# Kernel optimization log

Measured on AMD Instinct MI355X. Metric: run time of the kernel, lower is better.

The kernel has to match this reference:

```python
import jax, jax.numpy as jnp
import numpy as np

MASK_VALUE = -10000000000.0
B, S = 2, 2048
HQ, HKV, HD = 16, 8, 256
D = HQ * HD  # 4096
ROPE_BASE = 10000.0


def rms_norm(x, scale, eps=1e-6):
    # Gemma-style RMSNorm over the last (head_dim) axis with (1 + scale) gain.
    var = jnp.mean(jnp.square(x), axis=-1, keepdims=True)
    return x * jax.lax.rsqrt(var + eps) * (1.0 + scale)


def apply_rope(x, positions):
    # x: [b, t, h, d]; positions: [b, t]
    d = x.shape[-1]
    fraction = 2.0 * jnp.arange(d // 2, dtype=jnp.float32) / d
    timescale = ROPE_BASE ** fraction                     # [d/2]
    sinusoid = positions[..., None].astype(jnp.float32) / timescale  # [b, t, d/2]
    sin = jnp.sin(sinusoid)[:, :, None, :]                # [b, t, 1, d/2]
    cos = jnp.cos(sinusoid)[:, :, None, :]
    first, second = jnp.split(x, 2, axis=-1)
    out = jnp.concatenate([first * cos - second * sin,
                           second * cos + first * sin], axis=-1)
    return out.astype(x.dtype)


def setup_inputs() -> dict:
    key = jax.random.key(0)
    ks = jax.random.split(key, 6)
    x = jax.random.normal(ks[0], (B, S, D), dtype=jnp.float32)
    Wq = jax.random.normal(ks[1], (D, HQ * HD), dtype=jnp.float32) * 0.02
    Wk = jax.random.normal(ks[2], (D, HKV * HD), dtype=jnp.float32) * 0.02
    Wv = jax.random.normal(ks[3], (D, HKV * HD), dtype=jnp.float32) * 0.02
    Wo = jax.random.normal(ks[4], (HQ * HD, D), dtype=jnp.float32) * 0.02
    k_scale = jnp.zeros((HD,), dtype=jnp.float32)
    v_scale = jnp.zeros((HD,), dtype=jnp.float32)
    mask = jnp.broadcast_to(jnp.tril(jnp.ones((S, S), dtype=bool))[None], (B, S, S))
    position = jnp.broadcast_to(jnp.arange(S, dtype=jnp.int32)[None], (B, S))
    return {"x": x, "Wq": Wq, "Wk": Wk, "Wv": Wv, "Wo": Wo,
            "k_scale": k_scale, "v_scale": v_scale,
            "mask": mask, "position": position}


def reference(x, Wq, Wk, Wv, Wo, k_scale, v_scale, mask, position):
    b, t, _ = x.shape
    group = HQ // HKV
    q = (x @ Wq).reshape(b, t, HQ, HD)
    k = (x @ Wk).reshape(b, t, HKV, HD)
    v = (x @ Wv).reshape(b, t, HKV, HD)
    k = rms_norm(k, k_scale)
    v = rms_norm(v, v_scale)
    q = apply_rope(q, position)
    k = apply_rope(k, position)
    # [b, hkv, group, t, d] view of q; avoids materializing repeated K/V (same math as repeat).
    q = q.transpose(0, 2, 1, 3).reshape(b, HKV, group, t, HD)
    k = k.transpose(0, 2, 1, 3)  # [b, hkv, T, d]
    v = v.transpose(0, 2, 1, 3)
    scores = jnp.einsum('bhgtd,bhTd->bhgtT', q, k) / jnp.sqrt(jnp.float32(HD))
    scores = jnp.where(mask[:, None, None, :, :], scores, MASK_VALUE)
    weights = jax.nn.softmax(scores, axis=-1)
    out = jnp.einsum('bhgtT,bhTd->bhgtd', weights, v)
    out = out.reshape(b, HQ, t, HD).transpose(0, 2, 1, 3).reshape(b, t, HQ * HD)
    return out @ Wo
```

## Files before the change

kernel.cpp:

```cpp
#include <hip/hip_runtime.h>
#include <stdint.h>

typedef __bf16 bf16;
typedef __bf16 bf16x4 __attribute__((ext_vector_type(4)));
typedef __bf16 bf16x8 __attribute__((ext_vector_type(8)));
typedef float f32x4 __attribute__((ext_vector_type(4)));

#define GAS __attribute__((address_space(1)))
#define LAS __attribute__((address_space(3)))

__device__ __forceinline__ void gload_lds16(const void* g, void* l) {
  __builtin_amdgcn_global_load_lds((GAS const void*)g, (LAS void*)l, 16, 0, 0);
}

__global__ __launch_bounds__(256) void cvt_bf16(const float* __restrict__ in,
                                                bf16* __restrict__ out, int n4) {
  int i = blockIdx.x * 256 + threadIdx.x;
  if (i >= n4) return;
  float4 v = ((const float4*)in)[i];
  bf16x4 o;
  o[0] = (bf16)v.x; o[1] = (bf16)v.y; o[2] = (bf16)v.z; o[3] = (bf16)v.w;
  ((bf16x4*)out)[i] = o;
}

__global__ __launch_bounds__(256) void tconv(const float* __restrict__ W,
                                             bf16* __restrict__ Wt, int K, int N) {
  __shared__ bf16 tile[64][65];
  const int tx = threadIdx.x & 63, ty = threadIdx.x >> 6;
  const int n0 = blockIdx.x * 64, k0 = blockIdx.y * 64;
#pragma unroll
  for (int i = 0; i < 16; ++i) {
    int kr = ty + i * 4;
    tile[kr][tx] = (bf16)W[(size_t)(k0 + kr) * N + n0 + tx];
  }
  __syncthreads();
#pragma unroll
  for (int i = 0; i < 16; ++i) {
    int nr = ty + i * 4;
    Wt[(size_t)(n0 + nr) * K + k0 + tx] = tile[tx][nr];
  }
}

template <int OUTF32>
__global__ __launch_bounds__(256, 3) void gemm_bt(const bf16* __restrict__ A,
                                                  const bf16* __restrict__ Bt,
                                                  void* __restrict__ Cp,
                                                  const int M, const int N, const int K) {
  __shared__ __attribute__((aligned(16))) bf16 As[4096];
  __shared__ __attribute__((aligned(16))) bf16 Bs[4096];
  const int t = threadIdx.x, w = t >> 6, l = t & 63;
  const int la = l & 15, lq = l >> 4;
  const int m0 = blockIdx.y * 128, n0 = blockIdx.x * 128;
  const int wr = w >> 1, wc = w & 1;
  const int r1 = t >> 2, s1 = (t & 3) ^ (r1 & 3);
  const bf16* Ag1 = A + (size_t)(m0 + r1) * K + s1 * 8;
  const bf16* Ag2 = A + (size_t)(m0 + r1 + 64) * K + s1 * 8;
  const bf16* Bg1 = Bt + (size_t)(n0 + r1) * K + s1 * 8;
  const bf16* Bg2 = Bt + (size_t)(n0 + r1 + 64) * K + s1 * 8;
  const int rdsl = (lq ^ (la & 3)) << 3;

  f32x4 acc[4][4] = {};

  for (int kt = 0; kt < K; kt += 32) {
    gload_lds16(Ag1 + kt, As + w * 512);
    gload_lds16(Ag2 + kt, As + 2048 + w * 512);
    gload_lds16(Bg1 + kt, Bs + w * 512);
    gload_lds16(Bg2 + kt, Bs + 2048 + w * 512);
    __syncthreads();
    bf16x8 af[4], bfr[4];
#pragma unroll
    for (int i = 0; i < 4; ++i) {
      af[i] = *(const bf16x8*)(As + (wr * 64 + i * 16 + la) * 32 + rdsl);
      bfr[i] = *(const bf16x8*)(Bs + (wc * 64 + i * 16 + la) * 32 + rdsl);
    }
#pragma unroll
    for (int mi = 0; mi < 4; ++mi)
#pragma unroll
      for (int ni = 0; ni < 4; ++ni)
        acc[mi][ni] = __builtin_amdgcn_mfma_f32_16x16x32_bf16(af[mi], bfr[ni], acc[mi][ni], 0, 0, 0);
    __syncthreads();
  }

  const int crow = m0 + wr * 64, ccol = n0 + wc * 64;
  if (OUTF32) {
    float* C = (float*)Cp;
#pragma unroll
    for (int mi = 0; mi < 4; ++mi)
#pragma unroll
      for (int ni = 0; ni < 4; ++ni)
#pragma unroll
        for (int i = 0; i < 4; ++i)
          C[(size_t)(crow + mi * 16 + lq * 4 + i) * N + ccol + ni * 16 + la] = acc[mi][ni][i];
  } else {
    bf16* C = (bf16*)Cp;
#pragma unroll
    for (int mi = 0; mi < 4; ++mi)
#pragma unroll
      for (int ni = 0; ni < 4; ++ni)
#pragma unroll
        for (int i = 0; i < 4; ++i)
          C[(size_t)(crow + mi * 16 + lq * 4 + i) * N + ccol + ni * 16 + la] = (bf16)acc[mi][ni][i];
  }
}

__global__ __launch_bounds__(256) void rope_q(bf16* __restrict__ qq, const int* __restrict__ pos) {
  const int w = threadIdx.x >> 6, l = threadIdx.x & 63;
  const int row = blockIdx.x * 4 + w;
  const int bt = row >> 4;
  bf16* p = qq + (size_t)row * 256 + l * 4;
  bf16x4 xv = *(const bf16x4*)p;
  float x[4], y[4];
#pragma unroll
  for (int j = 0; j < 4; ++j) x[j] = (float)xv[j];
#pragma unroll
  for (int j = 0; j < 4; ++j) y[j] = __shfl_xor(x[j], 32, 64);
  const float posf = (float)pos[bt];
  bf16x4 ov;
#pragma unroll
  for (int j = 0; j < 4; ++j) {
    const int pr = (l & 31) * 4 + j;
    float sv, cv;
    sincosf(posf * exp2f((float)pr * (-13.287712379549449f / 128.0f)), &sv, &cv);
    float o = x[j] * cv + ((l < 32) ? -y[j] : y[j]) * sv;
    ov[j] = (bf16)(o * 0.0625f);
  }
  *(bf16x4*)p = ov;
}

__global__ __launch_bounds__(256) void norm_rope_k(bf16* __restrict__ kk,
                                                   const float* __restrict__ scale,
                                                   const int* __restrict__ pos) {
  const int w = threadIdx.x >> 6, l = threadIdx.x & 63;
  const int row = blockIdx.x * 4 + w;
  const int bt = row >> 3;
  bf16* p = kk + (size_t)row * 256 + l * 4;
  bf16x4 xv = *(const bf16x4*)p;
  float x[4];
#pragma unroll
  for (int j = 0; j < 4; ++j) x[j] = (float)xv[j];
  float ss = x[0] * x[0] + x[1] * x[1] + x[2] * x[2] + x[3] * x[3];
#pragma unroll
  for (int m = 1; m < 64; m <<= 1) ss += __shfl_xor(ss, m, 64);
  const float r = rsqrtf(ss * (1.0f / 256.0f) + 1e-6f);
#pragma unroll
  for (int j = 0; j < 4; ++j) x[j] = x[j] * r * (1.0f + scale[l * 4 + j]);
  float y[4];
#pragma unroll
  for (int j = 0; j < 4; ++j) y[j] = __shfl_xor(x[j], 32, 64);
  const float posf = (float)pos[bt];
  bf16x4 ov;
#pragma unroll
  for (int j = 0; j < 4; ++j) {
    const int pr = (l & 31) * 4 + j;
    float sv, cv;
    sincosf(posf * exp2f((float)pr * (-13.287712379549449f / 128.0f)), &sv, &cv);
    float o = x[j] * cv + ((l < 32) ? -y[j] : y[j]) * sv;
    ov[j] = (bf16)o;
  }
  *(bf16x4*)p = ov;
}

__global__ __launch_bounds__(256) void norm_v(bf16* __restrict__ vv,
                                              const float* __restrict__ scale) {
  const int w = threadIdx.x >> 6, l = threadIdx.x & 63;
  const int row = blockIdx.x * 4 + w;
  bf16* p = vv + (size_t)row * 256 + l * 4;
  bf16x4 xv = *(const bf16x4*)p;
  float x[4];
#pragma unroll
  for (int j = 0; j < 4; ++j) x[j] = (float)xv[j];
  float ss = x[0] * x[0] + x[1] * x[1] + x[2] * x[2] + x[3] * x[3];
#pragma unroll
  for (int m = 1; m < 64; m <<= 1) ss += __shfl_xor(ss, m, 64);
  const float r = rsqrtf(ss * (1.0f / 256.0f) + 1e-6f);
  bf16x4 ov;
#pragma unroll
  for (int j = 0; j < 4; ++j) ov[j] = (bf16)(x[j] * r * (1.0f + scale[l * 4 + j]));
  *(bf16x4*)p = ov;
}

__global__ __launch_bounds__(256) void vtrans(const bf16* __restrict__ v,
                                              bf16* __restrict__ vt) {
  __shared__ bf16 tile[64][65];
  const int tx = threadIdx.x & 63, ty = threadIdx.x >> 6;
  const int tt = blockIdx.x, dd = blockIdx.y, bh = blockIdx.z;
  const int b = bh >> 3, h = bh & 7;
#pragma unroll
  for (int i = 0; i < 16; ++i) {
    int trow = tt * 64 + ty + i * 4;
    tile[ty + i * 4][tx] = v[((size_t)(b * 2048 + trow) * 8 + h) * 256 + dd * 64 + tx];
  }
  __syncthreads();
#pragma unroll
  for (int i = 0; i < 16; ++i) {
    int drow = dd * 64 + ty + i * 4;
    vt[((size_t)(b * 8 + h) * 256 + drow) * 2048 + tt * 64 + tx] = tile[tx][ty + i * 4];
  }
}

__global__ __launch_bounds__(512, 2) void flash_attn(const bf16* __restrict__ q,
                                                     const bf16* __restrict__ k,
                                                     const bf16* __restrict__ vt,
                                                     bf16* __restrict__ o) {
  __shared__ __attribute__((aligned(16))) bf16 Ks[2 * 16384];
  __shared__ __attribute__((aligned(16))) bf16 Vs[2 * 16384];
  __shared__ __attribute__((aligned(16))) bf16 Ps[8 * 1152];
  const int t = threadIdx.x, w = t >> 6, l = t & 63;
  const int la = l & 15, lq = l >> 4;
  const int h = blockIdx.x, qbp = blockIdx.y, b = blockIdx.z;
  const int hkv = h >> 1;

  const bf16* kbase = k + (size_t)b * 2048 * 2048 + hkv * 256;
  const bf16* vbase = vt + ((size_t)(b * 8 + hkv)) * 256 * 2048;

  const bf16* ksrc[4];
  const bf16* vsrc[4];
#pragma unroll
  for (int i = 0; i < 4; ++i) {
    int c = i * 512 + t;
    int krr = c >> 5, ksl = (c & 31) ^ (krr & 7);
    int vrr = c >> 3, vsl = (c & 7) ^ (vrr & 7);
    ksrc[i] = kbase + (size_t)krr * 2048 + ksl * 8;
    vsrc[i] = vbase + (size_t)vrr * 2048 + vsl * 8;
  }

#define STAGE(bb, tt0)                                                        \
  do {                                                                        \
    _Pragma("unroll") for (int i_ = 0; i_ < 4; ++i_)                          \
        gload_lds16(ksrc[i_] + (size_t)(tt0) * 2048,                          \
                    Ks + (bb) * 16384 + i_ * 4096 + w * 512);                 \
    _Pragma("unroll") for (int i_ = 0; i_ < 4; ++i_)                          \
        gload_lds16(vsrc[i_] + (tt0), Vs + (bb) * 16384 + i_ * 4096 + w * 512); \
  } while (0)

  for (int part = 0; part < 2; ++part) {
    const int qb = part ? qbp : (15 - qbp);
    const int q0 = qb * 128;
    const int rbase = q0 + w * 16;

    bf16x8 qf[8];
    {
      const bf16* qrow = q + ((size_t)((b * 2048 + rbase + la) * 16 + h)) * 256 + lq * 8;
#pragma unroll
      for (int kg = 0; kg < 8; ++kg) qf[kg] = *(const bf16x8*)(qrow + kg * 32);
    }
    f32x4 acc[16] = {};
    float mrow[4] = {-1e30f, -1e30f, -1e30f, -1e30f};
    float lrow[4] = {0.f, 0.f, 0.f, 0.f};
    const int nT = 2 * qb + 2;

    STAGE(0, 0);
    int cur = 0;
    for (int tti = 0; tti < nT; ++tti) {
      const int t0 = tti * 64;
      if (tti + 1 < nT) {
        STAGE(cur ^ 1, t0 + 64);
        asm volatile("s_waitcnt vmcnt(8)" ::: "memory");
      } else {
        asm volatile("s_waitcnt vmcnt(0)" ::: "memory");
      }
      __builtin_amdgcn_s_barrier();
      __builtin_amdgcn_sched_barrier(0);
      if (t0 <= rbase + 15) {
        const bf16* Kc = Ks + cur * 16384;
        const bf16* Vc = Vs + cur * 16384;
        f32x4 s[4] = {};
        __builtin_amdgcn_s_setprio(1);
#pragma unroll
        for (int n = 0; n < 4; ++n) {
          int rT = n * 16 + la;
#pragma unroll
          for (int kg = 0; kg < 8; ++kg) {
            int sl = (kg * 4 + lq) ^ (rT & 7);
            bf16x8 kbv = *(const bf16x8*)(Kc + rT * 256 + sl * 8);
            s[n] = __builtin_amdgcn_mfma_f32_16x16x32_bf16(qf[kg], kbv, s[n], 0, 0, 0);
          }
        }
        __builtin_amdgcn_s_setprio(0);
        float scalef[4];
#pragma unroll
        for (int i = 0; i < 4; ++i) {
          const int row = rbase + lq * 4 + i;
          float mx = -1e30f;
#pragma unroll
          for (int n = 0; n < 4; ++n) {
            float v = s[n][i];
            v = (t0 + n * 16 + la > row) ? -1e30f : v;
            s[n][i] = v;
            mx = fmaxf(mx, v);
          }
          mx = fmaxf(mx, __shfl_xor(mx, 1, 64));
          mx = fmaxf(mx, __shfl_xor(mx, 2, 64));
          mx = fmaxf(mx, __shfl_xor(mx, 4, 64));
          mx = fmaxf(mx, __shfl_xor(mx, 8, 64));
          const float mnew = fmaxf(mrow[i], mx);
          scalef[i] = __expf(mrow[i] - mnew);
          float ps = 0.f;
#pragma unroll
          for (int n = 0; n < 4; ++n) {
            float v = s[n][i];
            float pp = (v <= -1e29f) ? 0.f : __expf(v - mnew);
            s[n][i] = pp;
            ps += pp;
          }
          ps += __shfl_xor(ps, 1, 64);
          ps += __shfl_xor(ps, 2, 64);
          ps += __shfl_xor(ps, 4, 64);
          ps += __shfl_xor(ps, 8, 64);
          mrow[i] = mnew;
          lrow[i] = lrow[i] * scalef[i] + ps;
        }
#pragma unroll
        for (int n = 0; n < 16; ++n) {
          acc[n][0] *= scalef[0]; acc[n][1] *= scalef[1];
          acc[n][2] *= scalef[2]; acc[n][3] *= scalef[3];
        }
        bf16* pw = Ps + w * 1152;
#pragma unroll
        for (int n = 0; n < 4; ++n)
#pragma unroll
          for (int i = 0; i < 4; ++i)
            pw[(lq * 4 + i) * 72 + n * 16 + la] = (bf16)s[n][i];
        __builtin_amdgcn_s_setprio(1);
#pragma unroll
        for (int kc = 0; kc < 2; ++kc) {
          bf16x8 pa = *(const bf16x8*)(pw + la * 72 + kc * 32 + lq * 8);
#pragma unroll
          for (int n = 0; n < 16; ++n) {
            int rd = n * 16 + la;
            int sl = (kc * 4 + lq) ^ (rd & 7);
            bf16x8 vbv = *(const bf16x8*)(Vc + rd * 64 + sl * 8);
            acc[n] = __builtin_amdgcn_mfma_f32_16x16x32_bf16(pa, vbv, acc[n], 0, 0, 0);
          }
        }
        __builtin_amdgcn_s_setprio(0);
      }
      __builtin_amdgcn_s_barrier();
      __builtin_amdgcn_sched_barrier(0);
      cur ^= 1;
    }
#pragma unroll
    for (int i = 0; i < 4; ++i) {
      const int row = rbase + lq * 4 + i;
      const float inv = 1.0f / lrow[i];
      bf16* orow = o + ((size_t)(b * 2048 + row)) * 4096 + h * 256;
#pragma unroll
      for (int n = 0; n < 16; ++n) orow[n * 16 + la] = (bf16)(acc[n][i] * inv);
    }
  }
#undef STAGE
}

__global__ void fill_err(float* o, int n) {
  int i = blockIdx.x * 256 + threadIdx.x;
  if (i < n) o[i] = 1e9f;
}

extern "C" void kernel_launch(void* const* d_in, const int* in_sizes, int n_in,
                              void* d_out, int out_size, void* d_ws, size_t ws_size,
                              hipStream_t stream) {
  const float* x = (const float*)d_in[0];
  const float* Wq = (const float*)d_in[1];
  const float* Wk = (const float*)d_in[2];
  const float* Wv = (const float*)d_in[3];
  const float* Wo = (const float*)d_in[4];
  const float* kscale = (const float*)d_in[5];
  const float* vscale = (const float*)d_in[6];
  const int* pos = (const int*)d_in[8];
  float* out = (float*)d_out;

  const size_t WS_NEED = 251658240ull;
  if (ws_size < WS_NEED) {
    fill_err<<<65536, 256, 0, stream>>>(out, out_size);
    return;
  }
  char* ws = (char*)d_ws;
  bf16* x16 = (bf16*)(ws);
  bf16* wqt = (bf16*)(ws + 33554432);
  bf16* wkt = (bf16*)(ws + 67108864);
  bf16* wvt = (bf16*)(ws + 83886080);
  bf16* wot = (bf16*)(ws + 100663296);
  bf16* qb = (bf16*)(ws + 134217728);
  bf16* kb = (bf16*)(ws + 167772160);
  bf16* vb = (bf16*)(ws + 184549376);
  bf16* vtb = (bf16*)(ws + 201326592);
  bf16* ao = (bf16*)(ws + 218103808);

  cvt_bf16<<<16384, 256, 0, stream>>>(x, x16, 4194304);
  tconv<<<dim3(64, 64), 256, 0, stream>>>(Wq, wqt, 4096, 4096);
  tconv<<<dim3(32, 64), 256, 0, stream>>>(Wk, wkt, 4096, 2048);
  tconv<<<dim3(32, 64), 256, 0, stream>>>(Wv, wvt, 4096, 2048);
  tconv<<<dim3(64, 64), 256, 0, stream>>>(Wo, wot, 4096, 4096);

  gemm_bt<0><<<dim3(32, 32), 256, 0, stream>>>(x16, wqt, qb, 4096, 4096, 4096);
  gemm_bt<0><<<dim3(16, 32), 256, 0, stream>>>(x16, wkt, kb, 4096, 2048, 4096);
  gemm_bt<0><<<dim3(16, 32), 256, 0, stream>>>(x16, wvt, vb, 4096, 2048, 4096);

  rope_q<<<16384, 256, 0, stream>>>(qb, pos);
  norm_rope_k<<<8192, 256, 0, stream>>>(kb, kscale, pos);
  norm_v<<<8192, 256, 0, stream>>>(vb, vscale);
  vtrans<<<dim3(32, 4, 16), 256, 0, stream>>>(vb, vtb);

  flash_attn<<<dim3(16, 8, 2), 512, 0, stream>>>(qb, kb, vtb, ao);

  gemm_bt<1><<<dim3(32, 32), 256, 0, stream>>>(ao, wot, out, 4096, 4096, 4096);
}
```

Baseline: 744.0 us.

## Fuse QKV projections into one GEMM with 256x256 pipelined tiles

Concatenates the transposed Wq/Wk/Wv into one weight matrix so a single GEMM produces an interleaved QKV buffer. The downstream rope, norm, transpose and attention kernels are re-indexed to read that layout. The GEMM is rewritten with 256x256 tiles, 512 threads, double-buffered LDS, and staged prefetch of the next K slab interleaved with MFMA phases. It also adds XCD-aware block swizzling and setprio. The aim is more data reuse per tile, fewer launches and overlap of loads with compute, at the cost of higher LDS and register use per block.

Result: faster. 666.7 us (-10.4%).

```diff
diff --git a/kernel.cpp b/kernel.cpp
--- a/kernel.cpp
+++ b/kernel.cpp
@@ -42,50 +42,98 @@
 }
 
 template <int OUTF32>
-__global__ __launch_bounds__(256, 3) void gemm_bt(const bf16* __restrict__ A,
+__global__ __launch_bounds__(512, 2) void gemm256(const bf16* __restrict__ A,
                                                   const bf16* __restrict__ Bt,
                                                   void* __restrict__ Cp,
-                                                  const int M, const int N, const int K) {
-  __shared__ __attribute__((aligned(16))) bf16 As[4096];
-  __shared__ __attribute__((aligned(16))) bf16 Bs[4096];
+                                                  const int N, const int K,
+                                                  const int NBX) {
+  __shared__ __attribute__((aligned(16))) bf16 lds[2][4][8192];
   const int t = threadIdx.x, w = t >> 6, l = t & 63;
   const int la = l & 15, lq = l >> 4;
-  const int m0 = blockIdx.y * 128, n0 = blockIdx.x * 128;
-  const int wr = w >> 1, wc = w & 1;
-  const int r1 = t >> 2, s1 = (t & 3) ^ (r1 & 3);
-  const bf16* Ag1 = A + (size_t)(m0 + r1) * K + s1 * 8;
-  const bf16* Ag2 = A + (size_t)(m0 + r1 + 64) * K + s1 * 8;
-  const bf16* Bg1 = Bt + (size_t)(n0 + r1) * K + s1 * 8;
-  const bf16* Bg2 = Bt + (size_t)(n0 + r1 + 64) * K + s1 * 8;
-  const int rdsl = (lq ^ (la & 3)) << 3;
-
-  f32x4 acc[4][4] = {};
-
-  for (int kt = 0; kt < K; kt += 32) {
-    gload_lds16(Ag1 + kt, As + w * 512);
-    gload_lds16(Ag2 + kt, As + 2048 + w * 512);
-    gload_lds16(Bg1 + kt, Bs + w * 512);
-    gload_lds16(Bg2 + kt, Bs + 2048 + w * 512);
-    __syncthreads();
-    bf16x8 af[4], bfr[4];
-#pragma unroll
-    for (int i = 0; i < 4; ++i) {
-      af[i] = *(const bf16x8*)(As + (wr * 64 + i * 16 + la) * 32 + rdsl);
-      bfr[i] = *(const bf16x8*)(Bs + (wc * 64 + i * 16 + la) * 32 + rdsl);
-    }
-#pragma unroll
-    for (int mi = 0; mi < 4; ++mi)
-#pragma unroll
-      for (int ni = 0; ni < 4; ++ni)
-        acc[mi][ni] = __builtin_amdgcn_mfma_f32_16x16x32_bf16(af[mi], bfr[ni], acc[mi][ni], 0, 0, 0);
-    __syncthreads();
-  }
-
-  const int crow = m0 + wr * 64, ccol = n0 + wc * 64;
+  const int nwg = gridDim.x, cpx = nwg >> 3;
+  const int sid = (blockIdx.x & 7) * cpx + (blockIdx.x >> 3);
+  const int by = sid / NBX, bx = sid % NBX;
+  const int m0 = by * 256, n0 = bx * 256;
+  const int wr = w >> 2, wc = w & 3;
+  const int c0 = w * 64 + l;
+  const int sr0 = c0 >> 2, soff = (((c0 & 3) ^ ((c0 >> 3) & 3)) << 3);
+  const bf16* pA0 = A + (size_t)(m0 + sr0) * K + soff;
+  const bf16* pA1 = pA0 + (size_t)128 * K;
+  const bf16* pB0 = Bt + (size_t)(n0 + sr0) * K + soff;
+  const bf16* pB1 = pB0 + (size_t)128 * K;
+  const int rsl = (lq ^ ((la >> 1) & 3)) << 3;
+
+  f32x4 acc[8][4] = {};
+
+#define STAGE_SLAB(s, nb, kti)                                                \
+  do {                                                                        \
+    const bf16* p0_ = ((s) & 1) ? pB0 : pA0;                                  \
+    const bf16* p1_ = ((s) & 1) ? pB1 : pA1;                                  \
+    const size_t ko_ = (size_t)(kti) * 64 + ((s) >> 1) * 32;                  \
+    gload_lds16(p0_ + ko_, &lds[nb][s][w * 512]);                             \
+    gload_lds16(p1_ + ko_, &lds[nb][s][4096 + w * 512]);                      \
+  } while (0)
+
+#define PHASE(kh, mg, LOADB)                                                  \
+  {                                                                           \
+    bf16x8 a_[4];                                                             \
+    _Pragma("unroll") for (int m_ = 0; m_ < 4; ++m_)                          \
+        a_[m_] = *(const bf16x8*)&lds[bi][(kh)*2][(wr * 128 + (mg)*64 + m_ * 16 + la) * 32 + rsl]; \
+    if (LOADB) {                                                              \
+      _Pragma("unroll") for (int n_ = 0; n_ < 4; ++n_)                        \
+          bfr[n_] = *(const bf16x8*)&lds[bi][(kh)*2 + 1][(wc * 64 + n_ * 16 + la) * 32 + rsl]; \
+    }                                                                         \
+    __builtin_amdgcn_s_setprio(1);                                            \
+    _Pragma("unroll") for (int m_ = 0; m_ < 4; ++m_)                          \
+      _Pragma("unroll") for (int n_ = 0; n_ < 4; ++n_)                        \
+          acc[(mg)*4 + m_][n_] = __builtin_amdgcn_mfma_f32_16x16x32_bf16(     \
+              a_[m_], bfr[n_], acc[(mg)*4 + m_][n_], 0, 0, 0);                \
+    __builtin_amdgcn_s_setprio(0);                                            \
+  }
+
+  STAGE_SLAB(0, 0, 0);
+  STAGE_SLAB(1, 0, 0);
+  STAGE_SLAB(2, 0, 0);
+  STAGE_SLAB(3, 0, 0);
+
+  const int NT = K >> 6;
+  for (int kt = 0; kt < NT; ++kt) {
+    const int bi = kt & 1, nbi = bi ^ 1;
+    const bool pf = (kt + 1) < NT;
+    bf16x8 bfr[4];
+    if (pf) asm volatile("s_waitcnt vmcnt(4)" ::: "memory");
+    else    asm volatile("s_waitcnt vmcnt(0)" ::: "memory");
+    __builtin_amdgcn_s_barrier();
+    __builtin_amdgcn_sched_barrier(0);
+    if (pf) STAGE_SLAB(0, nbi, kt + 1);
+    PHASE(0, 0, 1)
+    __builtin_amdgcn_s_barrier();
+    __builtin_amdgcn_sched_barrier(0);
+    if (pf) STAGE_SLAB(1, nbi, kt + 1);
+    PHASE(0, 1, 0)
+    __builtin_amdgcn_s_barrier();
+    __builtin_amdgcn_sched_barrier(0);
+    if (pf) asm volatile("s_waitcnt vmcnt(4)" ::: "memory");
+    else    asm volatile("s_waitcnt vmcnt(0)" ::: "memory");
+    __builtin_amdgcn_s_barrier();
+    __builtin_amdgcn_sched_barrier(0);
+    if (pf) STAGE_SLAB(2, nbi, kt + 1);
+    PHASE(1, 0, 1)
+    __builtin_amdgcn_s_barrier();
+    __builtin_amdgcn_sched_barrier(0);
+    if (pf) STAGE_SLAB(3, nbi, kt + 1);
+    PHASE(1, 1, 0)
+    __builtin_amdgcn_s_barrier();
+    __builtin_amdgcn_sched_barrier(0);
+  }
+#undef PHASE
+#undef STAGE_SLAB
+
+  const int crow = m0 + wr * 128, ccol = n0 + wc * 64;
   if (OUTF32) {
     float* C = (float*)Cp;
 #pragma unroll
-    for (int mi = 0; mi < 4; ++mi)
+    for (int mi = 0; mi < 8; ++mi)
 #pragma unroll
       for (int ni = 0; ni < 4; ++ni)
 #pragma unroll
@@ -94,7 +142,7 @@
   } else {
     bf16* C = (bf16*)Cp;
 #pragma unroll
-    for (int mi = 0; mi < 4; ++mi)
+    for (int mi = 0; mi < 8; ++mi)
 #pragma unroll
       for (int ni = 0; ni < 4; ++ni)
 #pragma unroll
@@ -103,11 +151,11 @@
   }
 }
 
-__global__ __launch_bounds__(256) void rope_q(bf16* __restrict__ qq, const int* __restrict__ pos) {
+__global__ __launch_bounds__(256) void rope_q(bf16* __restrict__ qkv, const int* __restrict__ pos) {
   const int w = threadIdx.x >> 6, l = threadIdx.x & 63;
-  const int row = blockIdx.x * 4 + w;
-  const int bt = row >> 4;
-  bf16* p = qq + (size_t)row * 256 + l * 4;
+  const int idx = blockIdx.x * 4 + w;
+  const int bt = idx >> 4, h = idx & 15;
+  bf16* p = qkv + (size_t)bt * 8192 + h * 256 + l * 4;
   bf16x4 xv = *(const bf16x4*)p;
   float x[4], y[4];
 #pragma unroll
@@ -127,13 +175,13 @@
   *(bf16x4*)p = ov;
 }
 
-__global__ __launch_bounds__(256) void norm_rope_k(bf16* __restrict__ kk,
+__global__ __launch_bounds__(256) void norm_rope_k(bf16* __restrict__ kbase,
                                                    const float* __restrict__ scale,
                                                    const int* __restrict__ pos) {
   const int w = threadIdx.x >> 6, l = threadIdx.x & 63;
-  const int row = blockIdx.x * 4 + w;
-  const int bt = row >> 3;
-  bf16* p = kk + (size_t)row * 256 + l * 4;
+  const int idx = blockIdx.x * 4 + w;
+  const int bt = idx >> 3, h = idx & 7;
+  bf16* p = kbase + (size_t)bt * 8192 + h * 256 + l * 4;
   bf16x4 xv = *(const bf16x4*)p;
   float x[4];
 #pragma unroll
@@ -160,11 +208,12 @@
   *(bf16x4*)p = ov;
 }
 
-__global__ __launch_bounds__(256) void norm_v(bf16* __restrict__ vv,
+__global__ __launch_bounds__(256) void norm_v(bf16* __restrict__ vbase,
                                               const float* __restrict__ scale) {
   const int w = threadIdx.x >> 6, l = threadIdx.x & 63;
-  const int row = blockIdx.x * 4 + w;
-  bf16* p = vv + (size_t)row * 256 + l * 4;
+  const int idx = blockIdx.x * 4 + w;
+  const int bt = idx >> 3, h = idx & 7;
+  bf16* p = vbase + (size_t)bt * 8192 + h * 256 + l * 4;
   bf16x4 xv = *(const bf16x4*)p;
   float x[4];
 #pragma unroll
@@ -179,7 +228,7 @@
   *(bf16x4*)p = ov;
 }
 
-__global__ __launch_bounds__(256) void vtrans(const bf16* __restrict__ v,
+__global__ __launch_bounds__(256) void vtrans(const bf16* __restrict__ vbase,
                                               bf16* __restrict__ vt) {
   __shared__ bf16 tile[64][65];
   const int tx = threadIdx.x & 63, ty = threadIdx.x >> 6;
@@ -188,7 +237,7 @@
 #pragma unroll
   for (int i = 0; i < 16; ++i) {
     int trow = tt * 64 + ty + i * 4;
-    tile[ty + i * 4][tx] = v[((size_t)(b * 2048 + trow) * 8 + h) * 256 + dd * 64 + tx];
+    tile[ty + i * 4][tx] = vbase[(size_t)(b * 2048 + trow) * 8192 + h * 256 + dd * 64 + tx];
   }
   __syncthreads();
 #pragma unroll
@@ -198,8 +247,7 @@
   }
 }
 
-__global__ __launch_bounds__(512, 2) void flash_attn(const bf16* __restrict__ q,
-                                                     const bf16* __restrict__ k,
+__global__ __launch_bounds__(512, 2) void flash_attn(const bf16* __restrict__ qkv,
                                                      const bf16* __restrict__ vt,
                                                      bf16* __restrict__ o) {
   __shared__ __attribute__((aligned(16))) bf16 Ks[2 * 16384];
@@ -210,7 +258,7 @@
   const int h = blockIdx.x, qbp = blockIdx.y, b = blockIdx.z;
   const int hkv = h >> 1;
 
-  const bf16* kbase = k + (size_t)b * 2048 * 2048 + hkv * 256;
+  const bf16* kbase = qkv + (size_t)(b * 2048) * 8192 + 4096 + hkv * 256;
   const bf16* vbase = vt + ((size_t)(b * 8 + hkv)) * 256 * 2048;
 
   const bf16* ksrc[4];
@@ -220,14 +268,14 @@
     int c = i * 512 + t;
     int krr = c >> 5, ksl = (c & 31) ^ (krr & 7);
     int vrr = c >> 3, vsl = (c & 7) ^ (vrr & 7);
-    ksrc[i] = kbase + (size_t)krr * 2048 + ksl * 8;
+    ksrc[i] = kbase + (size_t)krr * 8192 + ksl * 8;
     vsrc[i] = vbase + (size_t)vrr * 2048 + vsl * 8;
   }
 
 #define STAGE(bb, tt0)                                                        \
   do {                                                                        \
     _Pragma("unroll") for (int i_ = 0; i_ < 4; ++i_)                          \
-        gload_lds16(ksrc[i_] + (size_t)(tt0) * 2048,                          \
+        gload_lds16(ksrc[i_] + (size_t)(tt0) * 8192,                          \
                     Ks + (bb) * 16384 + i_ * 4096 + w * 512);                 \
     _Pragma("unroll") for (int i_ = 0; i_ < 4; ++i_)                          \
         gload_lds16(vsrc[i_] + (tt0), Vs + (bb) * 16384 + i_ * 4096 + w * 512); \
@@ -240,7 +288,7 @@
 
     bf16x8 qf[8];
     {
-      const bf16* qrow = q + ((size_t)((b * 2048 + rbase + la) * 16 + h)) * 256 + lq * 8;
+      const bf16* qrow = qkv + (size_t)(b * 2048 + rbase + la) * 8192 + h * 256 + lq * 8;
 #pragma unroll
       for (int kg = 0; kg < 8; ++kg) qf[kg] = *(const bf16x8*)(qrow + kg * 32);
     }
@@ -375,33 +423,27 @@
     return;
   }
   char* ws = (char*)d_ws;
-  bf16* x16 = (bf16*)(ws);
-  bf16* wqt = (bf16*)(ws + 33554432);
-  bf16* wkt = (bf16*)(ws + 67108864);
-  bf16* wvt = (bf16*)(ws + 83886080);
-  bf16* wot = (bf16*)(ws + 100663296);
-  bf16* qb = (bf16*)(ws + 134217728);
-  bf16* kb = (bf16*)(ws + 167772160);
-  bf16* vb = (bf16*)(ws + 184549376);
-  bf16* vtb = (bf16*)(ws + 201326592);
-  bf16* ao = (bf16*)(ws + 218103808);
+  bf16* x16   = (bf16*)(ws);
+  bf16* wqkvt = (bf16*)(ws + 33554432);
+  bf16* wot   = (bf16*)(ws + 100663296);
+  bf16* qkv   = (bf16*)(ws + 134217728);
+  bf16* vtb   = (bf16*)(ws + 201326592);
+  bf16* ao    = (bf16*)(ws + 218103808);
 
   cvt_bf16<<<16384, 256, 0, stream>>>(x, x16, 4194304);
-  tconv<<<dim3(64, 64), 256, 0, stream>>>(Wq, wqt, 4096, 4096);
-  tconv<<<dim3(32, 64), 256, 0, stream>>>(Wk, wkt, 4096, 2048);
-  tconv<<<dim3(32, 64), 256, 0, stream>>>(Wv, wvt, 4096, 2048);
+  tconv<<<dim3(64, 64), 256, 0, stream>>>(Wq, wqkvt, 4096, 4096);
+  tconv<<<dim3(32, 64), 256, 0, stream>>>(Wk, wqkvt + (size_t)4096 * 4096, 4096, 2048);
+  tconv<<<dim3(32, 64), 256, 0, stream>>>(Wv, wqkvt + (size_t)6144 * 4096, 4096, 2048);
   tconv<<<dim3(64, 64), 256, 0, stream>>>(Wo, wot, 4096, 4096);
 
-  gemm_bt<0><<<dim3(32, 32), 256, 0, stream>>>(x16, wqt, qb, 4096, 4096, 4096);
-  gemm_bt<0><<<dim3(16, 32), 256, 0, stream>>>(x16, wkt, kb, 4096, 2048, 4096);
-  gemm_bt<0><<<dim3(16, 32), 256, 0, stream>>>(x16, wvt, vb, 4096, 2048, 4096);
-
-  rope_q<<<16384, 256, 0, stream>>>(qb, pos);
-  norm_rope_k<<<8192, 256, 0, stream>>>(kb, kscale, pos);
-  norm_v<<<8192, 256, 0, stream>>>(vb, vscale);
-  vtrans<<<dim3(32, 4, 16), 256, 0, stream>>>(vb, vtb);
-
-  flash_attn<<<dim3(16, 8, 2), 512, 0, stream>>>(qb, kb, vtb, ao);
-
-  gemm_bt<1><<<dim3(32, 32), 256, 0, stream>>>(ao, wot, out, 4096, 4096, 4096);
-}
+  gemm256<0><<<512, 512, 0, stream>>>(x16, wqkvt, qkv, 8192, 4096, 32);
+
+  rope_q<<<16384, 256, 0, stream>>>(qkv, pos);
+  norm_rope_k<<<8192, 256, 0, stream>>>(qkv + 4096, kscale, pos);
+  norm_v<<<8192, 256, 0, stream>>>(qkv + 6144, vscale);
+  vtrans<<<dim3(32, 4, 16), 256, 0, stream>>>(qkv + 6144, vtb);
+
+  flash_attn<<<dim3(16, 8, 2), 512, 0, stream>>>(qkv, vtb, ao);
+
+  gemm256<1><<<256, 512, 0, stream>>>(ao, wot, out, 4096, 4096, 16);
+}
```
